# Optimization experiments

Measured on AMD Instinct MI355X. Metric: run time of the kernel, lower is better.

Reference implementation:

```python
import jax, jax.numpy as jnp
import numpy as np

B, L, K = 8, 512, 30
H, NUM_IN, NPTS = 128, 384, 8
EPS = 1e-8


def _linear_params(key, din, dout):
    kw, kb = jax.random.split(key)
    W = jax.random.normal(kw, (din, dout), jnp.float32) * 0.02
    b = jax.random.normal(kb, (dout,), jnp.float32) * 0.02
    return W, b


def setup_inputs() -> dict:
    key = jax.random.key(0)
    ks = jax.random.split(key, 10)
    h_V = jax.random.normal(ks[0], (B, L, H), jnp.float32)
    h_E = jax.random.normal(ks[1], (B, L, K, NUM_IN), jnp.float32)
    E_idx = jax.random.randint(ks[2], (B, L, K), 0, L)
    X_neighbors = jax.random.normal(ks[3], (B, L, K, 3, 3), jnp.float32) * 3.0
    mask_V = jnp.ones((B, L), jnp.float32)
    mask_attend = jnp.ones((B, L, K), jnp.float32)
    Wp, bp = _linear_params(ks[4], H, NPTS * 3)
    W1, b1 = _linear_params(ks[5], H + NUM_IN + 9 * NPTS, H)
    W2, b2 = _linear_params(ks[6], H, H)
    W3, b3 = _linear_params(ks[7], H, H)
    Wi, bi = _linear_params(ks[8], H, 4 * H)
    Wo, bo = _linear_params(ks[9], 4 * H, H)
    g1 = jnp.ones((H,), jnp.float32); be1 = jnp.zeros((H,), jnp.float32)
    g2 = jnp.ones((H,), jnp.float32); be2 = jnp.zeros((H,), jnp.float32)
    return dict(h_V=h_V, h_E=h_E, E_idx=E_idx, X_neighbors=X_neighbors,
                mask_V=mask_V, mask_attend=mask_attend,
                Wp=Wp, bp=bp, W1=W1, b1=b1, W2=W2, b2=b2, W3=W3, b3=b3,
                Wi=Wi, bi=bi, Wo=Wo, bo=bo, g1=g1, be1=be1, g2=g2, be2=be2)


def _frames(N, CA, C):
    # openfold Rigid.from_3_points (Gram-Schmidt): x-axis along CA-N, C in xy-plane
    e0 = CA - N
    e0 = e0 / jnp.sqrt(jnp.sum(e0 * e0, -1, keepdims=True) + EPS)
    e1 = C - CA
    e1 = e1 - e0 * jnp.sum(e0 * e1, -1, keepdims=True)
    e1 = e1 / jnp.sqrt(jnp.sum(e1 * e1, -1, keepdims=True) + EPS)
    e2 = jnp.cross(e0, e1)
    R = jnp.stack([e0, e1, e2], axis=-1)  # basis vectors as columns
    return R, CA


def _ln(x, g, b):
    m = jnp.mean(x, -1, keepdims=True)
    v = jnp.var(x, -1, keepdims=True)
    return (x - m) / jnp.sqrt(v + 1e-5) * g + b


def _forward(h_V, h_E, X_neighbors, mask_V, mask_attend, Wp, bp, W1, b1, W2, b2,
             W3, b3, Wi, bi, Wo, bo, g1, be1, g2, be2):
    gelu = lambda x: jax.nn.gelu(x, approximate=False)
    # per-neighbor backbone frames: [B,L,K,3,3], [B,L,K,3]
    R, t = _frames(X_neighbors[..., 0, :], X_neighbors[..., 1, :], X_neighbors[..., 2, :])
    h_V_prev = h_E[..., -H:]
    sh = h_E.shape[:-1]  # (B,L,K)
    p_ln = (h_V_prev @ Wp + bp).reshape(*sh, NPTS, 3)  # local points of each neighbor
    p_local = p_ln[:, :, 0]                            # [B,L,n,3] (self is neighbor 0)
    npg = jnp.einsum('blkij,blknj->blkni', R, p_ln) + t[..., None, :]  # global points
    p_global = npg[:, :, 0]
    pge = jnp.broadcast_to(p_global[:, :, None], npg.shape)
    ple = jnp.broadcast_to(p_local[:, :, None], npg.shape)
    pln = jnp.sqrt(jnp.sum(ple * ple, -1) + EPS)
    R0 = R[:, :, 0]; t0 = t[:, :, 0]  # self frame
    npl = jnp.einsum('blji,blknj->blkni', R0, npg - t0[:, :, None, None, :])  # invert_apply
    npl_norm = jnp.sqrt(jnp.sum(npl * npl, -1) + EPS)
    npg_norm = jnp.sqrt(jnp.sum((pge - npg) ** 2, -1) + EPS)
    node_expand = jnp.broadcast_to(h_V[:, :, None, :], (*sh, H))
    msg = jnp.concatenate([node_expand, h_E,
                           ple.reshape(*sh, -1), pln,
                           npl.reshape(*sh, -1), npl_norm, npg_norm], axis=-1)
    node_m = gelu(msg @ W1 + b1)
    node_m = gelu(node_m @ W2 + b2)
    node_m = node_m @ W3 + b3
    node_m = mask_attend[..., None] * node_m
    node_m = jnp.mean(node_m, axis=-2)
    h = _ln(h_V + node_m, g1, be1)  # dropout is identity in eval
    d = gelu(h @ Wi + bi) @ Wo + bo
    h = _ln(h + d, g2, be2)
    return mask_V[..., None] * h


def reference(h_V, h_E, E_idx, X_neighbors, mask_V, mask_attend, Wp, bp, W1, b1,
              W2, b2, W3, b3, Wi, bi, Wo, bo, g1, be1, g2, be2):
    # E_idx only defines the neighbor axis shape; geometry comes pre-gathered in X_neighbors/h_E
    return _forward(h_V, h_E, X_neighbors, mask_V, mask_attend, Wp, bp, W1, b1,
                    W2, b2, W3, b3, Wi, bi, Wo, bo, g1, be1, g2, be2)
```

## Files before the change

kernel.cpp:

```cpp
#include <hip/hip_runtime.h>

#define B_ 8
#define L_ 512
#define K_ 30
#define NIN_ 384
#define HES 11520
#define BUFW 136
#define GFW 96
#define PWU 4608
#define R0_OFF 0
#define T0_OFF 9
#define PL0_OFF 12
#define NPG_OFF 40
#define PLF_OFF 760
#define NM_OFF 640
#define GEOF_OFF 1520

typedef __attribute__((ext_vector_type(8))) short short8;
typedef __attribute__((ext_vector_type(8))) unsigned short ushort8;
typedef __attribute__((ext_vector_type(4))) float floatx4;
typedef __attribute__((ext_vector_type(4))) float f32x4;

__device__ __forceinline__ float b2f(unsigned short u) {
    union { unsigned int i; float f; } x; x.i = ((unsigned int)u) << 16; return x.f;
}
__device__ __forceinline__ unsigned short f2b(float f) {
    unsigned int u = __builtin_bit_cast(unsigned int, f);
    return (unsigned short)((u + 0x7fffu + ((u >> 16) & 1u)) >> 16);
}
__device__ __forceinline__ float gelu_f(float x) {
    return 0.5f * x * (1.0f + erff(x * 0.70710678118654752440f));
}
__device__ __forceinline__ short8 pack8(const float* p) {
    f32x4 lo = *(const f32x4*)p;
    f32x4 hi = *(const f32x4*)(p + 4);
    short8 r;
    r[0] = (short)f2b(lo[0]); r[1] = (short)f2b(lo[1]);
    r[2] = (short)f2b(lo[2]); r[3] = (short)f2b(lo[3]);
    r[4] = (short)f2b(hi[0]); r[5] = (short)f2b(hi[1]);
    r[6] = (short)f2b(hi[2]); r[7] = (short)f2b(hi[3]);
    return r;
}

__global__ __launch_bounds__(256) void prep_kernel(
        const float* __restrict__ W1, const float* __restrict__ W2,
        const float* __restrict__ W3, const float* __restrict__ Wi,
        const float* __restrict__ Wo, const float* __restrict__ Wp,
        unsigned short* __restrict__ ws) {
    __shared__ float T[64][65];
    int b = blockIdx.x, tid = threadIdx.x;
    const float* in; int K, N, NOUT, KP; size_t off; int kt, nt;
    if (b < 20)      { in = W1; K = 584; N = 128; NOUT = 128; KP = 608; off = 0;      kt = b / 2; nt = b % 2; }
    else if (b < 24) { b -= 20; in = W2; K = 128; N = 128; NOUT = 128; KP = 128; off = 77824;  kt = b / 2; nt = b % 2; }
    else if (b < 28) { b -= 24; in = W3; K = 128; N = 128; NOUT = 128; KP = 128; off = 94208;  kt = b / 2; nt = b % 2; }
    else if (b < 44) { b -= 28; in = Wi; K = 128; N = 512; NOUT = 512; KP = 128; off = 110592; kt = b / 8; nt = b % 8; }
    else if (b < 60) { b -= 44; in = Wo; K = 512; N = 128; NOUT = 128; KP = 512; off = 176128; kt = b % 8; nt = b / 8; }
    else             { b -= 60; in = Wp; K = 128; N = 24;  NOUT = 32;  KP = 128; off = 241664; kt = b;     nt = 0; }

    for (int t = 0; t < 16; ++t) {
        int idx = t * 256 + tid;
        int r = idx >> 6, c = idx & 63;
        int gk = kt * 64 + r, gn = nt * 64 + c;
        T[c][r] = (gk < K && gn < N) ? in[(size_t)gk * N + gn] : 0.0f;
    }
    __syncthreads();
    for (int t = 0; t < 2; ++t) {
        int j = t * 256 + tid;
        int orow = j >> 3, oseg = (j & 7) * 8;
        int gn = nt * 64 + orow, gk = kt * 64 + oseg;
        if (gn < NOUT && gk < KP) {
            ushort8 o8;
            for (int i = 0; i < 8; ++i) o8[i] = f2b(T[orow][oseg + i]);
            *(ushort8*)(ws + off + (size_t)gn * KP + gk) = o8;
        }
    }
}

__global__ __launch_bounds__(128, 4) void main_kernel(
    const float* __restrict__ h_V,
    const float* __restrict__ h_E,
    const float* __restrict__ Xn,
    const float* __restrict__ mask_V,
    const float* __restrict__ mask_attend,
    const float* __restrict__ bp,
    const float* __restrict__ b1g,
    const float* __restrict__ b2g,
    const float* __restrict__ b3g,
    const float* __restrict__ big,
    const float* __restrict__ bog,
    const float* __restrict__ g1,
    const float* __restrict__ be1,
    const float* __restrict__ g2,
    const float* __restrict__ be2,
    const unsigned short* __restrict__ wsT,
    float* __restrict__ out) {

    __shared__ __align__(16) unsigned short lds[2 * PWU];

    const int tid  = threadIdx.x;
    const int wv   = tid >> 6;
    const int lane = tid & 63;
    const int quad = lane >> 4;
    const int l16  = lane & 15;
    const int ko   = quad * 8;
    const int site = blockIdx.x * 2 + wv;

    unsigned short* wl   = lds + wv * PWU;
    unsigned short* buf1 = wl;
    unsigned short* geoF = wl + GEOF_OFF;
    float*          Fv   = (float*)wl;

    const unsigned short* W1T = wsT;
    const unsigned short* W2T = wsT + 77824;
    const unsigned short* W3T = wsT + 94208;
    const unsigned short* WiT = wsT + 110592;
    const unsigned short* WoT = wsT + 176128;
    const unsigned short* WpT = wsT + 241664;

    const float* hEb = h_E + (size_t)site * HES;
    const float* hVb = h_V + site * 128;
    const short8 z8 = {0, 0, 0, 0, 0, 0, 0, 0};

    float maskR[2][4];
    for (int rt = 0; rt < 2; ++rt)
        for (int r = 0; r < 4; ++r) {
            int row = rt * 16 + quad * 4 + r;
            maskR[rt][r] = (row < K_) ? mask_attend[site * K_ + row] * (1.0f / 30.0f) : 0.0f;
        }

    float Rr[9], Tt[3];
    if (lane < K_) {
        const float* xp = Xn + ((size_t)site * K_ + lane) * 9;
        float Nx = xp[0], Ny = xp[1], Nz = xp[2];
        float Ax = xp[3], Ay = xp[4], Az = xp[5];
        float Cx = xp[6], Cy = xp[7], Cz = xp[8];
        float e0x = Ax - Nx, e0y = Ay - Ny, e0z = Az - Nz;
        float r0 = 1.0f / sqrtf(e0x * e0x + e0y * e0y + e0z * e0z + 1e-8f);
        e0x *= r0; e0y *= r0; e0z *= r0;
        float u1x = Cx - Ax, u1y = Cy - Ay, u1z = Cz - Az;
        float d = e0x * u1x + e0y * u1y + e0z * u1z;
        u1x -= e0x * d; u1y -= e0y * d; u1z -= e0z * d;
        float r1 = 1.0f / sqrtf(u1x * u1x + u1y * u1y + u1z * u1z + 1e-8f);
        u1x *= r1; u1y *= r1; u1z *= r1;
        Rr[0] = e0x; Rr[1] = u1x; Rr[2] = e0y * u1z - e0z * u1y;
        Rr[3] = e0y; Rr[4] = u1y; Rr[5] = e0z * u1x - e0x * u1z;
        Rr[6] = e0z; Rr[7] = u1z; Rr[8] = e0x * u1y - e0y * u1x;
        Tt[0] = Ax; Tt[1] = Ay; Tt[2] = Az;
    }

    {
        floatx4 a[2][2] = {{{0,0,0,0},{0,0,0,0}},{{0,0,0,0},{0,0,0,0}}};
        for (int kc = 0; kc < 4; ++kc) {
            int col = 256 + kc * 32 + ko;
            short8 fa0 = pack8(hEb + l16 * NIN_ + col);
            int r1 = 16 + l16;
            short8 fa1 = (r1 < K_) ? pack8(hEb + r1 * NIN_ + col) : z8;
            for (int ct = 0; ct < 2; ++ct) {
                short8 fb = *(const short8*)(WpT + (ct * 16 + l16) * 128 + kc * 32 + ko);
                a[0][ct] = __builtin_amdgcn_mfma_f32_16x16x32_bf16(fa0, fb, a[0][ct], 0, 0, 0);
                a[1][ct] = __builtin_amdgcn_mfma_f32_16x16x32_bf16(fa1, fb, a[1][ct], 0, 0, 0);
            }
        }
        for (int ct = 0; ct < 2; ++ct) {
            int ccol = ct * 16 + l16;
            if (ccol < 24) {
                float bpc = bp[ccol];
                for (int rt = 0; rt < 2; ++rt)
                    for (int i = 0; i < 4; ++i) {
                        int row = rt * 16 + quad * 4 + i;
                        if (row < K_) Fv[PLF_OFF + row * 24 + ccol] = a[rt][ct][i] + bpc;
                    }
            }
        }
    }

    if (lane < K_) {
        float pl[24];
        #pragma unroll
        for (int c = 0; c < 24; ++c) pl[c] = Fv[PLF_OFF + lane * 24 + c];
        if (lane == 0) {
            #pragma unroll
            for (int i = 0; i < 9; ++i) Fv[R0_OFF + i] = Rr[i];
            Fv[T0_OFF] = Tt[0]; Fv[T0_OFF + 1] = Tt[1]; Fv[T0_OFF + 2] = Tt[2];
            #pragma unroll
            for (int c = 0; c < 24; ++c) Fv[PL0_OFF + c] = pl[c];
        }
        #pragma unroll
        for (int n = 0; n < 8; ++n) {
            float p0 = pl[n * 3], p1 = pl[n * 3 + 1], p2 = pl[n * 3 + 2];
            #pragma unroll
            for (int i = 0; i < 3; ++i)
                Fv[NPG_OFF + lane * 24 + n * 3 + i] =
                    Rr[i * 3 + 0] * p0 + Rr[i * 3 + 1] * p1 + Rr[i * 3 + 2] * p2 + Tt[i];
        }
    }

    for (int id = lane; id < 720; id += 64) geoF[(id / 24) * GFW + 72 + id % 24] = 0;
    {
        float R00 = Fv[0], R01 = Fv[1], R02 = Fv[2], R03 = Fv[3], R04 = Fv[4];
        float R05 = Fv[5], R06 = Fv[6], R07 = Fv[7], R08 = Fv[8];
        float T00 = Fv[9], T01 = Fv[10], T02 = Fv[11];
        for (int id = lane; id < 240; id += 64) {
            int k = id >> 3, n = id & 7;
            float p0 = Fv[PL0_OFF + n * 3], p1 = Fv[PL0_OFF + n * 3 + 1], p2 = Fv[PL0_OFF + n * 3 + 2];
            float q0g = Fv[NPG_OFF + n * 3], q1g = Fv[NPG_OFF + n * 3 + 1], q2g = Fv[NPG_OFF + n * 3 + 2];
            float a0 = Fv[NPG_OFF + k * 24 + n * 3];
            float a1 = Fv[NPG_OFF + k * 24 + n * 3 + 1];
            float a2 = Fv[NPG_OFF + k * 24 + n * 3 + 2];
            float d0 = a0 - T00, d1 = a1 - T01, d2 = a2 - T02;
            float nl0 = R00 * d0 + R03 * d1 + R06 * d2;
            float nl1 = R01 * d0 + R04 * d1 + R07 * d2;
            float nl2 = R02 * d0 + R05 * d1 + R08 * d2;
            unsigned short* gf = geoF + k * GFW;
            gf[0 + n * 3] = f2b(p0); gf[1 + n * 3] = f2b(p1); gf[2 + n * 3] = f2b(p2);
            gf[24 + n] = f2b(sqrtf(p0 * p0 + p1 * p1 + p2 * p2 + 1e-8f));
            gf[32 + n * 3] = f2b(nl0); gf[33 + n * 3] = f2b(nl1); gf[34 + n * 3] = f2b(nl2);
            gf[56 + n] = f2b(sqrtf(nl0 * nl0 + nl1 * nl1 + nl2 * nl2 + 1e-8f));
            float q0 = q0g - a0, q1 = q1g - a1, q2 = q2g - a2;
            gf[64 + n] = f2b(sqrtf(q0 * q0 + q1 * q1 + q2 * q2 + 1e-8f));
        }
    }

    {
        floatx4 acc[2][8];
        for (int rt = 0; rt < 2; ++rt) for (int ct = 0; ct < 8; ++ct) acc[rt][ct] = (floatx4){0,0,0,0};
        for (int kc = 0; kc < 4; ++kc) {
            int col = kc * 32 + ko;
            short8 fa = pack8(hVb + col);
            for (int ct = 0; ct < 8; ++ct) {
                short8 fb = *(const short8*)(W1T + (ct * 16 + l16) * 608 + col);
                acc[0][ct] = __builtin_amdgcn_mfma_f32_16x16x32_bf16(fa, fb, acc[0][ct], 0, 0, 0);
                acc[1][ct] = __builtin_amdgcn_mfma_f32_16x16x32_bf16(fa, fb, acc[1][ct], 0, 0, 0);
            }
        }
        for (int kc = 0; kc < 12; ++kc) {
            int col = kc * 32 + ko;
            short8 fa0 = pack8(hEb + l16 * NIN_ + col);
            int r1 = 16 + l16;
            short8 fa1 = (r1 < K_) ? pack8(hEb + r1 * NIN_ + col) : z8;
            for (int ct = 0; ct < 8; ++ct) {
                short8 fb = *(const short8*)(W1T + (ct * 16 + l16) * 608 + 128 + col);
                acc[0][ct] = __builtin_amdgcn_mfma_f32_16x16x32_bf16(fa0, fb, acc[0][ct], 0, 0, 0);
                acc[1][ct] = __builtin_amdgcn_mfma_f32_16x16x32_bf16(fa1, fb, acc[1][ct], 0, 0, 0);
            }
        }
        for (int kc = 0; kc < 3; ++kc) {
            int col = kc * 32 + ko;
            short8 fa0 = *(const short8*)&geoF[l16 * GFW + col];
            int r1 = 16 + l16;
            short8 fa1 = (r1 < K_) ? *(const short8*)&geoF[r1 * GFW + col] : z8;
            for (int ct = 0; ct < 8; ++ct) {
                short8 fb = *(const short8*)(W1T + (ct * 16 + l16) * 608 + 512 + col);
                acc[0][ct] = __builtin_amdgcn_mfma_f32_16x16x32_bf16(fa0, fb, acc[0][ct], 0, 0, 0);
                acc[1][ct] = __builtin_amdgcn_mfma_f32_16x16x32_bf16(fa1, fb, acc[1][ct], 0, 0, 0);
            }
        }
        for (int ct = 0; ct < 8; ++ct) {
            int col = ct * 16 + l16;
            float bb = b1g[col];
            for (int rt = 0; rt < 2; ++rt)
                for (int r = 0; r < 4; ++r) {
                    int row = rt * 16 + quad * 4 + r;
                    buf1[row * BUFW + col] = f2b(gelu_f(acc[rt][ct][r] + bb));
                }
        }
    }

    {
        short8 Af[2][4];
        for (int kc = 0; kc < 4; ++kc) {
            Af[0][kc] = *(const short8*)&buf1[l16 * BUFW + kc * 32 + ko];
            Af[1][kc] = *(const short8*)&buf1[(16 + l16) * BUFW + kc * 32 + ko];
        }
        floatx4 acc[2][8];
        for (int rt = 0; rt < 2; ++rt) for (int ct = 0; ct < 8; ++ct) acc[rt][ct] = (floatx4){0,0,0,0};
        for (int kc = 0; kc < 4; ++kc)
            for (int ct = 0; ct < 8; ++ct) {
                short8 fb = *(const short8*)(W2T + (ct * 16 + l16) * 128 + kc * 32 + ko);
                acc[0][ct] = __builtin_amdgcn_mfma_f32_16x16x32_bf16(Af[0][kc], fb, acc[0][ct], 0, 0, 0);
                acc[1][ct] = __builtin_amdgcn_mfma_f32_16x16x32_bf16(Af[1][kc], fb, acc[1][ct], 0, 0, 0);
            }
        for (int ct = 0; ct < 8; ++ct) {
            int col = ct * 16 + l16;
            float bb = b2g[col];
            for (int rt = 0; rt < 2; ++rt)
                for (int r = 0; r < 4; ++r) {
                    int row = rt * 16 + quad * 4 + r;
                    buf1[row * BUFW + col] = f2b(gelu_f(acc[rt][ct][r] + bb));
                }
        }
    }

    {
        short8 Af[2][4];
        for (int kc = 0; kc < 4; ++kc) {
            Af[0][kc] = *(const short8*)&buf1[l16 * BUFW + kc * 32 + ko];
            Af[1][kc] = *(const short8*)&buf1[(16 + l16) * BUFW + kc * 32 + ko];
        }
        floatx4 acc[2][8];
        for (int rt = 0; rt < 2; ++rt) for (int ct = 0; ct < 8; ++ct) acc[rt][ct] = (floatx4){0,0,0,0};
        for (int kc = 0; kc < 4; ++kc)
            for (int ct = 0; ct < 8; ++ct) {
                short8 fb = *(const short8*)(W3T + (ct * 16 + l16) * 128 + kc * 32 + ko);
                acc[0][ct] = __builtin_amdgcn_mfma_f32_16x16x32_bf16(Af[0][kc], fb, acc[0][ct], 0, 0, 0);
                acc[1][ct] = __builtin_amdgcn_mfma_f32_16x16x32_bf16(Af[1][kc], fb, acc[1][ct], 0, 0, 0);
            }
        for (int ct = 0; ct < 8; ++ct) {
            int col = ct * 16 + l16;
            float bb = b3g[col];
            float cs = 0.0f;
            for (int rt = 0; rt < 2; ++rt)
                for (int r = 0; r < 4; ++r)
                    cs += (acc[rt][ct][r] + bb) * maskR[rt][r];
            cs += __shfl_xor(cs, 16, 64);
            cs += __shfl_xor(cs, 32, 64);
            if (lane < 16) Fv[NM_OFF + col] = cs;
        }
    }

    {
        int c0 = lane, c1 = lane + 64;
        float xb0 = hVb[c0] + Fv[NM_OFF + c0];
        float xb1 = hVb[c1] + Fv[NM_OFF + c1];
        float s = xb0 + xb1, q = xb0 * xb0 + xb1 * xb1;
        for (int o = 32; o; o >>= 1) { s += __shfl_xor(s, o, 64); q += __shfl_xor(q, o, 64); }
        float m = s * (1.0f / 128.0f);
        float inv = 1.0f / sqrtf(q * (1.0f / 128.0f) - m * m + 1e-5f);
        float h0 = (xb0 - m) * inv * g1[c0] + be1[c0];
        float h1 = (xb1 - m) * inv * g1[c1] + be1[c1];
        Fv[c0] = h0; Fv[c1] = h1;

        for (int j = 0; j < 8; ++j) {
            int o = lane + 64 * j;
            const ushort8* wr = (const ushort8*)(WiT + o * 128);
            float sa = big[o], sb = 0.0f;
            for (int c8 = 0; c8 < 16; c8 += 2) {
                ushort8 v0 = wr[c8], v1 = wr[c8 + 1];
                const float* hp0 = &Fv[c8 * 8];
                const float* hp1 = &Fv[c8 * 8 + 8];
                sa += hp0[0] * b2f(v0[0]) + hp0[1] * b2f(v0[1]) + hp0[2] * b2f(v0[2]) + hp0[3] * b2f(v0[3]) +
                      hp0[4] * b2f(v0[4]) + hp0[5] * b2f(v0[5]) + hp0[6] * b2f(v0[6]) + hp0[7] * b2f(v0[7]);
                sb += hp1[0] * b2f(v1[0]) + hp1[1] * b2f(v1[1]) + hp1[2] * b2f(v1[2]) + hp1[3] * b2f(v1[3]) +
                      hp1[4] * b2f(v1[4]) + hp1[5] * b2f(v1[5]) + hp1[6] * b2f(v1[6]) + hp1[7] * b2f(v1[7]);
            }
            Fv[128 + o] = gelu_f(sa + sb);
        }

        float d0a = bog[c0], d0b = 0.0f, d1a = bog[c1], d1b = 0.0f;
        {
            const ushort8* w0 = (const ushort8*)(WoT + c0 * 512);
            const ushort8* w1 = (const ushort8*)(WoT + c1 * 512);
            for (int o8 = 0; o8 < 64; o8 += 2) {
                ushort8 v0 = w0[o8], v0n = w0[o8 + 1];
                ushort8 v1 = w1[o8], v1n = w1[o8 + 1];
                const float* gp = &Fv[128 + o8 * 8];
                const float* gq = gp + 8;
                d0a += gp[0] * b2f(v0[0]) + gp[1] * b2f(v0[1]) + gp[2] * b2f(v0[2]) + gp[3] * b2f(v0[3]) +
                       gp[4] * b2f(v0[4]) + gp[5] * b2f(v0[5]) + gp[6] * b2f(v0[6]) + gp[7] * b2f(v0[7]);
                d0b += gq[0] * b2f(v0n[0]) + gq[1] * b2f(v0n[1]) + gq[2] * b2f(v0n[2]) + gq[3] * b2f(v0n[3]) +
                       gq[4] * b2f(v0n[4]) + gq[5] * b2f(v0n[5]) + gq[6] * b2f(v0n[6]) + gq[7] * b2f(v0n[7]);
                d1a += gp[0] * b2f(v1[0]) + gp[1] * b2f(v1[1]) + gp[2] * b2f(v1[2]) + gp[3] * b2f(v1[3]) +
                       gp[4] * b2f(v1[4]) + gp[5] * b2f(v1[5]) + gp[6] * b2f(v1[6]) + gp[7] * b2f(v1[7]);
                d1b += gq[0] * b2f(v1n[0]) + gq[1] * b2f(v1n[1]) + gq[2] * b2f(v1n[2]) + gq[3] * b2f(v1n[3]) +
                       gq[4] * b2f(v1n[4]) + gq[5] * b2f(v1n[5]) + gq[6] * b2f(v1n[6]) + gq[7] * b2f(v1n[7]);
            }
        }
        float y0 = h0 + d0a + d0b, y1 = h1 + d1a + d1b;
        float s2 = y0 + y1, q2 = y0 * y0 + y1 * y1;
        for (int o = 32; o; o >>= 1) { s2 += __shfl_xor(s2, o, 64); q2 += __shfl_xor(q2, o, 64); }
        float m2 = s2 * (1.0f / 128.0f);
        float inv2 = 1.0f / sqrtf(q2 * (1.0f / 128.0f) - m2 * m2 + 1e-5f);
        float mv = mask_V[site];
        out[site * 128 + c0] = ((y0 - m2) * inv2 * g2[c0] + be2[c0]) * mv;
        out[site * 128 + c1] = ((y1 - m2) * inv2 * g2[c1] + be2[c1]) * mv;
    }
}

extern "C" void kernel_launch(void* const* d_in, const int* in_sizes, int n_in,
                              void* d_out, int out_size, void* d_ws, size_t ws_size,
                              hipStream_t stream) {
    const float* h_V = (const float*)d_in[0];
    const float* h_E = (const float*)d_in[1];
    const float* Xn  = (const float*)d_in[3];
    const float* mV  = (const float*)d_in[4];
    const float* mA  = (const float*)d_in[5];
    const float* Wp  = (const float*)d_in[6];
    const float* bp  = (const float*)d_in[7];
    const float* W1  = (const float*)d_in[8];
    const float* b1  = (const float*)d_in[9];
    const float* W2  = (const float*)d_in[10];
    const float* b2  = (const float*)d_in[11];
    const float* W3  = (const float*)d_in[12];
    const float* b3  = (const float*)d_in[13];
    const float* Wi  = (const float*)d_in[14];
    const float* bi  = (const float*)d_in[15];
    const float* Wo  = (const float*)d_in[16];
    const float* bo  = (const float*)d_in[17];
    const float* g1  = (const float*)d_in[18];
    const float* be1 = (const float*)d_in[19];
    const float* g2  = (const float*)d_in[20];
    const float* be2 = (const float*)d_in[21];
    unsigned short* ws = (unsigned short*)d_ws;
    float* out = (float*)d_out;

    prep_kernel<<<62, 256, 0, stream>>>(W1, W2, W3, Wi, Wo, Wp, ws);
    main_kernel<<<(B_ * L_) / 2, 128, 0, stream>>>(h_V, h_E, Xn, mV, mA, bp,
                                                   b1, b2, b3, bi, bo,
                                                   g1, be1, g2, be2, ws, out);
}
```

Measured before the change: 541.5 us.

## Pre-swizzle weights into MFMA fragment order for coalesced loads

The prep kernel now writes W1/W2/W3/Wp in per-fragment order, so each lane loads its B-operand short8 as one contiguous 16-byte chunk from a 1 KB block. Wi/Wo are rearranged so the per-output GEMV reads are coalesced across lanes instead of strided rows. The prep kernel moves from an LDS transpose to one element per thread over 960 blocks. Launch bounds drop from 4 to 3 waves-per-EU minimum, which gives the compiler more registers but may lower occupancy.

```diff
diff --git a/kernel.cpp b/kernel.cpp
--- a/kernel.cpp
+++ b/kernel.cpp
@@ -16,6 +16,13 @@
 #define NM_OFF 640
 #define GEOF_OFF 1520
 
+#define W1F_OFF 0
+#define W2F_OFF 77824
+#define W3F_OFF 94208
+#define WIF_OFF 110592
+#define WOF_OFF 176128
+#define WPF_OFF 241664
+
 typedef __attribute__((ext_vector_type(8))) short short8;
 typedef __attribute__((ext_vector_type(8))) unsigned short ushort8;
 typedef __attribute__((ext_vector_type(4))) float floatx4;
@@ -41,42 +48,49 @@
     r[6] = (short)f2b(hi[2]); r[7] = (short)f2b(hi[3]);
     return r;
 }
+__device__ __forceinline__ float dot8(const float* hp, ushort8 v) {
+    return hp[0] * b2f(v[0]) + hp[1] * b2f(v[1]) + hp[2] * b2f(v[2]) + hp[3] * b2f(v[3]) +
+           hp[4] * b2f(v[4]) + hp[5] * b2f(v[5]) + hp[6] * b2f(v[6]) + hp[7] * b2f(v[7]);
+}
 
 __global__ __launch_bounds__(256) void prep_kernel(
         const float* __restrict__ W1, const float* __restrict__ W2,
         const float* __restrict__ W3, const float* __restrict__ Wi,
         const float* __restrict__ Wo, const float* __restrict__ Wp,
         unsigned short* __restrict__ ws) {
-    __shared__ float T[64][65];
-    int b = blockIdx.x, tid = threadIdx.x;
-    const float* in; int K, N, NOUT, KP; size_t off; int kt, nt;
-    if (b < 20)      { in = W1; K = 584; N = 128; NOUT = 128; KP = 608; off = 0;      kt = b / 2; nt = b % 2; }
-    else if (b < 24) { b -= 20; in = W2; K = 128; N = 128; NOUT = 128; KP = 128; off = 77824;  kt = b / 2; nt = b % 2; }
-    else if (b < 28) { b -= 24; in = W3; K = 128; N = 128; NOUT = 128; KP = 128; off = 94208;  kt = b / 2; nt = b % 2; }
-    else if (b < 44) { b -= 28; in = Wi; K = 128; N = 512; NOUT = 512; KP = 128; off = 110592; kt = b / 8; nt = b % 8; }
-    else if (b < 60) { b -= 44; in = Wo; K = 512; N = 128; NOUT = 128; KP = 512; off = 176128; kt = b % 8; nt = b / 8; }
-    else             { b -= 60; in = Wp; K = 128; N = 24;  NOUT = 32;  KP = 128; off = 241664; kt = b;     nt = 0; }
-
-    for (int t = 0; t < 16; ++t) {
-        int idx = t * 256 + tid;
-        int r = idx >> 6, c = idx & 63;
-        int gk = kt * 64 + r, gn = nt * 64 + c;
-        T[c][r] = (gk < K && gn < N) ? in[(size_t)gk * N + gn] : 0.0f;
-    }
-    __syncthreads();
-    for (int t = 0; t < 2; ++t) {
-        int j = t * 256 + tid;
-        int orow = j >> 3, oseg = (j & 7) * 8;
-        int gn = nt * 64 + orow, gk = kt * 64 + oseg;
-        if (gn < NOUT && gk < KP) {
-            ushort8 o8;
-            for (int i = 0; i < 8; ++i) o8[i] = f2b(T[orow][oseg + i]);
-            *(ushort8*)(ws + off + (size_t)gn * KP + gk) = o8;
-        }
-    }
-}
-
-__global__ __launch_bounds__(128, 4) void main_kernel(
+    int idx = blockIdx.x * 256 + threadIdx.x;
+    if (idx < 94208 || (idx >= 241664 && idx < 245760)) {
+        const float* in; int i, KC, Kreal, Nreal, Nld;
+        if (idx < 77824)      { in = W1; i = idx;          KC = 19; Kreal = 584; Nreal = 128; Nld = 128; }
+        else if (idx < 94208) { in = W2; i = idx - 77824;  KC = 4;  Kreal = 128; Nreal = 128; Nld = 128; }
+        else                  { in = Wp; i = idx - 241664; KC = 4;  Kreal = 128; Nreal = 24;  Nld = 24;  }
+        int f = i >> 9, r = i & 511;
+        int ct = f / KC, kc = f % KC;
+        int lane = r >> 3, j = r & 7;
+        int q = lane >> 4, l = lane & 15;
+        int k = kc * 32 + q * 8 + j, n = ct * 16 + l;
+        ws[idx] = (k < Kreal && n < Nreal) ? f2b(in[k * Nld + n]) : (unsigned short)0;
+    } else if (idx < 110592) {
+        int i = idx - 94208;
+        int f = i >> 9, r = i & 511;
+        int ct = f >> 2, kc = f & 3;
+        int lane = r >> 3, j = r & 7;
+        int q = lane >> 4, l = lane & 15;
+        ws[idx] = f2b(W3[(kc * 32 + q * 8 + j) * 128 + ct * 16 + l]);
+    } else if (idx < 176128) {
+        int i = idx - 110592;
+        int c8 = i >> 12, r = i & 4095;
+        int o = r >> 3, ii = r & 7;
+        ws[idx] = f2b(Wi[(c8 * 8 + ii) * 512 + o]);
+    } else if (idx < 241664) {
+        int i = idx - 176128;
+        int o8 = i >> 10, r = i & 1023;
+        int c = r >> 3, ii = r & 7;
+        ws[idx] = f2b(Wo[(o8 * 8 + ii) * 128 + c]);
+    }
+}
+
+__global__ __launch_bounds__(128, 3) void main_kernel(
     const float* __restrict__ h_V,
     const float* __restrict__ h_E,
     const float* __restrict__ Xn,
@@ -110,12 +124,12 @@
     unsigned short* geoF = wl + GEOF_OFF;
     float*          Fv   = (float*)wl;
 
-    const unsigned short* W1T = wsT;
-    const unsigned short* W2T = wsT + 77824;
-    const unsigned short* W3T = wsT + 94208;
-    const unsigned short* WiT = wsT + 110592;
-    const unsigned short* WoT = wsT + 176128;
-    const unsigned short* WpT = wsT + 241664;
+    const unsigned short* W1F = wsT + W1F_OFF;
+    const unsigned short* W2F = wsT + W2F_OFF;
+    const unsigned short* W3F = wsT + W3F_OFF;
+    const unsigned short* WiF = wsT + WIF_OFF;
+    const unsigned short* WoF = wsT + WOF_OFF;
+    const unsigned short* WpF = wsT + WPF_OFF;
 
     const float* hEb = h_E + (size_t)site * HES;
     const float* hVb = h_V + site * 128;
@@ -156,7 +170,7 @@
             int r1 = 16 + l16;
             short8 fa1 = (r1 < K_) ? pack8(hEb + r1 * NIN_ + col) : z8;
             for (int ct = 0; ct < 2; ++ct) {
-                short8 fb = *(const short8*)(WpT + (ct * 16 + l16) * 128 + kc * 32 + ko);
+                short8 fb = *(const short8*)(WpF + (ct * 4 + kc) * 512 + lane * 8);
                 a[0][ct] = __builtin_amdgcn_mfma_f32_16x16x32_bf16(fa0, fb, a[0][ct], 0, 0, 0);
                 a[1][ct] = __builtin_amdgcn_mfma_f32_16x16x32_bf16(fa1, fb, a[1][ct], 0, 0, 0);
             }
@@ -228,7 +242,7 @@
             int col = kc * 32 + ko;
             short8 fa = pack8(hVb + col);
             for (int ct = 0; ct < 8; ++ct) {
-                short8 fb = *(const short8*)(W1T + (ct * 16 + l16) * 608 + col);
+                short8 fb = *(const short8*)(W1F + (ct * 19 + kc) * 512 + lane * 8);
                 acc[0][ct] = __builtin_amdgcn_mfma_f32_16x16x32_bf16(fa, fb, acc[0][ct], 0, 0, 0);
                 acc[1][ct] = __builtin_amdgcn_mfma_f32_16x16x32_bf16(fa, fb, acc[1][ct], 0, 0, 0);
             }
@@ -239,7 +253,7 @@
             int r1 = 16 + l16;
             short8 fa1 = (r1 < K_) ? pack8(hEb + r1 * NIN_ + col) : z8;
             for (int ct = 0; ct < 8; ++ct) {
-                short8 fb = *(const short8*)(W1T + (ct * 16 + l16) * 608 + 128 + col);
+                short8 fb = *(const short8*)(W1F + (ct * 19 + 4 + kc) * 512 + lane * 8);
                 acc[0][ct] = __builtin_amdgcn_mfma_f32_16x16x32_bf16(fa0, fb, acc[0][ct], 0, 0, 0);
                 acc[1][ct] = __builtin_amdgcn_mfma_f32_16x16x32_bf16(fa1, fb, acc[1][ct], 0, 0, 0);
             }
@@ -250,7 +264,7 @@
             int r1 = 16 + l16;
             short8 fa1 = (r1 < K_) ? *(const short8*)&geoF[r1 * GFW + col] : z8;
             for (int ct = 0; ct < 8; ++ct) {
-                short8 fb = *(const short8*)(W1T + (ct * 16 + l16) * 608 + 512 + col);
+                short8 fb = *(const short8*)(W1F + (ct * 19 + 16 + kc) * 512 + lane * 8);
                 acc[0][ct] = __builtin_amdgcn_mfma_f32_16x16x32_bf16(fa0, fb, acc[0][ct], 0, 0, 0);
                 acc[1][ct] = __builtin_amdgcn_mfma_f32_16x16x32_bf16(fa1, fb, acc[1][ct], 0, 0, 0);
             }
@@ -276,7 +290,7 @@
         for (int rt = 0; rt < 2; ++rt) for (int ct = 0; ct < 8; ++ct) acc[rt][ct] = (floatx4){0,0,0,0};
         for (int kc = 0; kc < 4; ++kc)
             for (int ct = 0; ct < 8; ++ct) {
-                short8 fb = *(const short8*)(W2T + (ct * 16 + l16) * 128 + kc * 32 + ko);
+                short8 fb = *(const short8*)(W2F + (ct * 4 + kc) * 512 + lane * 8);
                 acc[0][ct] = __builtin_amdgcn_mfma_f32_16x16x32_bf16(Af[0][kc], fb, acc[0][ct], 0, 0, 0);
                 acc[1][ct] = __builtin_amdgcn_mfma_f32_16x16x32_bf16(Af[1][kc], fb, acc[1][ct], 0, 0, 0);
             }
@@ -301,7 +315,7 @@
         for (int rt = 0; rt < 2; ++rt) for (int ct = 0; ct < 8; ++ct) acc[rt][ct] = (floatx4){0,0,0,0};
         for (int kc = 0; kc < 4; ++kc)
             for (int ct = 0; ct < 8; ++ct) {
-                short8 fb = *(const short8*)(W3T + (ct * 16 + l16) * 128 + kc * 32 + ko);
+                short8 fb = *(const short8*)(W3F + (ct * 4 + kc) * 512 + lane * 8);
                 acc[0][ct] = __builtin_amdgcn_mfma_f32_16x16x32_bf16(Af[0][kc], fb, acc[0][ct], 0, 0, 0);
                 acc[1][ct] = __builtin_amdgcn_mfma_f32_16x16x32_bf16(Af[1][kc], fb, acc[1][ct], 0, 0, 0);
             }
@@ -332,38 +346,25 @@
 
         for (int j = 0; j < 8; ++j) {
             int o = lane + 64 * j;
-            const ushort8* wr = (const ushort8*)(WiT + o * 128);
             float sa = big[o], sb = 0.0f;
             for (int c8 = 0; c8 < 16; c8 += 2) {
-                ushort8 v0 = wr[c8], v1 = wr[c8 + 1];
-                const float* hp0 = &Fv[c8 * 8];
-                const float* hp1 = &Fv[c8 * 8 + 8];
-                sa += hp0[0] * b2f(v0[0]) + hp0[1] * b2f(v0[1]) + hp0[2] * b2f(v0[2]) + hp0[3] * b2f(v0[3]) +
-                      hp0[4] * b2f(v0[4]) + hp0[5] * b2f(v0[5]) + hp0[6] * b2f(v0[6]) + hp0[7] * b2f(v0[7]);
-                sb += hp1[0] * b2f(v1[0]) + hp1[1] * b2f(v1[1]) + hp1[2] * b2f(v1[2]) + hp1[3] * b2f(v1[3]) +
-                      hp1[4] * b2f(v1[4]) + hp1[5] * b2f(v1[5]) + hp1[6] * b2f(v1[6]) + hp1[7] * b2f(v1[7]);
+                ushort8 v0 = *(const ushort8*)(WiF + c8 * 4096 + o * 8);
+                ushort8 v1 = *(const ushort8*)(WiF + (c8 + 1) * 4096 + o * 8);
+                sa += dot8(&Fv[c8 * 8], v0);
+                sb += dot8(&Fv[c8 * 8 + 8], v1);
             }
             Fv[128 + o] = gelu_f(sa + sb);
         }
 
         float d0a = bog[c0], d0b = 0.0f, d1a = bog[c1], d1b = 0.0f;
-        {
-            const ushort8* w0 = (const ushort8*)(WoT + c0 * 512);
-            const ushort8* w1 = (const ushort8*)(WoT + c1 * 512);
-            for (int o8 = 0; o8 < 64; o8 += 2) {
-                ushort8 v0 = w0[o8], v0n = w0[o8 + 1];
-                ushort8 v1 = w1[o8], v1n = w1[o8 + 1];
-                const float* gp = &Fv[128 + o8 * 8];
-                const float* gq = gp + 8;
-                d0a += gp[0] * b2f(v0[0]) + gp[1] * b2f(v0[1]) + gp[2] * b2f(v0[2]) + gp[3] * b2f(v0[3]) +
-                       gp[4] * b2f(v0[4]) + gp[5] * b2f(v0[5]) + gp[6] * b2f(v0[6]) + gp[7] * b2f(v0[7]);
-                d0b += gq[0] * b2f(v0n[0]) + gq[1] * b2f(v0n[1]) + gq[2] * b2f(v0n[2]) + gq[3] * b2f(v0n[3]) +
-                       gq[4] * b2f(v0n[4]) + gq[5] * b2f(v0n[5]) + gq[6] * b2f(v0n[6]) + gq[7] * b2f(v0n[7]);
-                d1a += gp[0] * b2f(v1[0]) + gp[1] * b2f(v1[1]) + gp[2] * b2f(v1[2]) + gp[3] * b2f(v1[3]) +
-                       gp[4] * b2f(v1[4]) + gp[5] * b2f(v1[5]) + gp[6] * b2f(v1[6]) + gp[7] * b2f(v1[7]);
-                d1b += gq[0] * b2f(v1n[0]) + gq[1] * b2f(v1n[1]) + gq[2] * b2f(v1n[2]) + gq[3] * b2f(v1n[3]) +
-                       gq[4] * b2f(v1n[4]) + gq[5] * b2f(v1n[5]) + gq[6] * b2f(v1n[6]) + gq[7] * b2f(v1n[7]);
-            }
+        for (int o8 = 0; o8 < 64; o8 += 2) {
+            ushort8 v0  = *(const ushort8*)(WoF + o8 * 1024 + c0 * 8);
+            ushort8 v0n = *(const ushort8*)(WoF + (o8 + 1) * 1024 + c0 * 8);
+            ushort8 v1  = *(const ushort8*)(WoF + o8 * 1024 + c1 * 8);
+            ushort8 v1n = *(const ushort8*)(WoF + (o8 + 1) * 1024 + c1 * 8);
+            const float* gp = &Fv[128 + o8 * 8];
+            d0a += dot8(gp, v0);  d0b += dot8(gp + 8, v0n);
+            d1a += dot8(gp, v1);  d1b += dot8(gp + 8, v1n);
         }
         float y0 = h0 + d0a + d0b, y1 = h1 + d1a + d1b;
         float s2 = y0 + y1, q2 = y0 * y0 + y1 * y1;
@@ -403,7 +404,7 @@
     unsigned short* ws = (unsigned short*)d_ws;
     float* out = (float*)d_out;
 
-    prep_kernel<<<62, 256, 0, stream>>>(W1, W2, W3, Wi, Wo, Wp, ws);
+    prep_kernel<<<960, 256, 0, stream>>>(W1, W2, W3, Wi, Wo, Wp, ws);
     main_kernel<<<(B_ * L_) / 2, 128, 0, stream>>>(h_V, h_E, Xn, mV, mA, bp,
                                                    b1, b2, b3, bi, bo,
                                                    g1, be1, g2, be2, ws, out);
```

After: 444.6 us. 1.22x faster.
